# Optimization experiments

Hardware: AMD Instinct MI355X
Metric: run time of the kernel (lower is better)

The kernel has to match this reference:

```python
import jax, jax.numpy as jnp
import numpy as np

H = 16      # numHeads (== numKeyValueHeads since keyValueHeadsPerHead=1)
D = 128     # headDim


def setup_inputs() -> dict:
    key = jax.random.key(0)
    k1, k2, k3 = jax.random.split(key, 3)
    B, S, dim = 2, 2048, 2048
    x = jax.random.normal(k1, (B, S, dim), dtype=jnp.float32)
    # qkvProj: Linear(dim -> (H + 2*H)*D) without bias; torch Linear weight is [out, in]
    Wqkv = jax.random.normal(k2, ((H + 2 * H) * D, dim), dtype=jnp.float32) * 0.02
    # outProj: Linear(H*D -> dim) without bias
    Wout = jax.random.normal(k3, (dim, H * D), dtype=jnp.float32) * 0.02
    return {"x": x, "Wqkv": Wqkv, "Wout": Wout}


def reference(x, Wqkv, Wout):
    B, S, _ = x.shape
    qkv = jnp.einsum('bsd,ed->bse', x, Wqkv)           # [B, S, 3*H*D]
    qkv = qkv.reshape(B, S, 3 * H, D)
    q = qkv[:, :, :H]                                  # [B, S, H, D]
    k = qkv[:, :, H:2 * H]                             # [B, S, H, D]
    v = qkv[:, :, 2 * H:]                              # [B, S, H, D]
    # explicit QK^T / sqrt(d), softmax in fp32, then @ V (keyValueHeadsPerHead=1
    # collapses the group axis, leaving standard per-head attention)
    logits = jnp.einsum('bqhd,bkhd->bhqk', q, k) * (D ** -0.5)
    w = jax.nn.softmax(logits.astype(jnp.float32), axis=-1).astype(logits.dtype)
    out = jnp.einsum('bhqk,bkhd->bqhd', w, v).reshape(B, S, H * D)
    return jnp.einsum('bse,de->bsd', out, Wout)        # outProj
```

## Files before the change

### kernel.cpp

```cpp
#include <hip/hip_runtime.h>

typedef __bf16 bf16x8 __attribute__((ext_vector_type(8)));
typedef _Float16 f16;
typedef f16 f16x8 __attribute__((ext_vector_type(8)));
typedef float f32x4 __attribute__((ext_vector_type(4)));
typedef unsigned short u16;
typedef u16 u16x4 __attribute__((ext_vector_type(4)));

__device__ __forceinline__ u16 f2bf(float f) {
  unsigned u = __builtin_bit_cast(unsigned, f);
  u += 0x7FFFu + ((u >> 16) & 1u);
  return (u16)(u >> 16);
}

#define GLDS16(g, l) __builtin_amdgcn_global_load_lds(                     \
    (const __attribute__((address_space(1))) unsigned int*)(g),            \
    (__attribute__((address_space(3))) unsigned int*)(l), 16, 0, 0)

__device__ __forceinline__ f32x4 mfma16(bf16x8 a, bf16x8 b, f32x4 c) {
  return __builtin_amdgcn_mfma_f32_16x16x32_bf16(a, b, c, 0, 0, 0);
}
__device__ __forceinline__ f32x4 mfma16h(f16x8 a, f16x8 b, f32x4 c) {
  return __builtin_amdgcn_mfma_f32_16x16x32_f16(a, b, c, 0, 0, 0);
}

__global__ void cvt_bf16(const float* __restrict__ src, u16* __restrict__ dst,
                         int n4, int n4s, float scale) {
  int idx = blockIdx.x * blockDim.x + threadIdx.x;
  int stride = gridDim.x * blockDim.x;
  for (int i = idx; i < n4; i += stride) {
    float4 v = ((const float4*)src)[i];
    float sc = (i < n4s) ? scale : 1.0f;
    u16x4 o = { f2bf(v.x * sc), f2bf(v.y * sc), f2bf(v.z * sc), f2bf(v.w * sc) };
    ((u16x4*)dst)[i] = o;
  }
}

__global__ __launch_bounds__(512, 1) void gemm1_qkv(
    const u16* __restrict__ A, const u16* __restrict__ B,
    u16* __restrict__ QK, u16* __restrict__ VT) {
  __shared__ __align__(16) u16 LA[2][16384];
  __shared__ __align__(16) u16 LB[2][16384];
  constexpr int K = 2048;
  const int t = threadIdx.x, lane = t & 63, w = t >> 6;
  const int wm = w >> 2, wn = w & 3;
  const int l15 = lane & 15, lg = lane >> 4;
  const int l7 = l15 & 7;

  const int bid = blockIdx.x;
  const int wg = (bid & 7) * 48 + (bid >> 3);
  const int bx = wg % 24, by = wg / 24;
  const int m0 = by * 256, n0 = bx * 256;

  const int srow = t >> 3;
  const int schunk = (t & 7) ^ (srow & 7);
  const u16* ga = A + (size_t)(m0 + srow) * K + schunk * 8;
  const u16* gb = B + (size_t)(n0 + srow) * K + schunk * 8;

  f32x4 acc[8][4] = {};

#define STG_ALL(kt, bf) do {                                               \
    const int ko_ = (kt) * 64;                                             \
    GLDS16(ga + ko_,            &LA[bf][0]     + t * 8);                   \
    GLDS16(ga + ko_ + 64  * K,  &LA[bf][4096]  + t * 8);                   \
    GLDS16(ga + ko_ + 128 * K,  &LA[bf][8192]  + t * 8);                   \
    GLDS16(ga + ko_ + 192 * K,  &LA[bf][12288] + t * 8);                   \
    GLDS16(gb + ko_,            &LB[bf][0]     + t * 8);                   \
    GLDS16(gb + ko_ + 64  * K,  &LB[bf][4096]  + t * 8);                   \
    GLDS16(gb + ko_ + 128 * K,  &LB[bf][8192]  + t * 8);                   \
    GLDS16(gb + ko_ + 192 * K,  &LB[bf][12288] + t * 8);                   \
  } while (0)
#define BAR() do { __builtin_amdgcn_s_barrier();                           \
                   __builtin_amdgcn_sched_barrier(0); } while (0)

  STG_ALL(0, 0);

#pragma unroll 1
  for (int T = 0; T < 32; ++T) {
    const int bf = T & 1;
    if (T < 31) {
      STG_ALL(T + 1, bf ^ 1);
      asm volatile("s_waitcnt vmcnt(8)" ::: "memory");
    } else {
      asm volatile("s_waitcnt vmcnt(0)" ::: "memory");
    }
    __builtin_amdgcn_sched_barrier(0);
    BAR();

    const u16* la = &LA[bf][0];
    const u16* lb = &LB[bf][0];
    bf16x8 aF[2][4], bF0[2][2], bF1[2][2];

#pragma unroll
    for (int kk = 0; kk < 2; ++kk) {
      const int cp = ((kk * 4 + lg) ^ l7) * 8;
#pragma unroll
      for (int i = 0; i < 4; ++i)
        aF[kk][i] = *(const bf16x8*)&la[(wm * 128 + i * 16 + l15) * 64 + cp];
#pragma unroll
      for (int j = 0; j < 2; ++j)
        bF0[kk][j] = *(const bf16x8*)&lb[(wn * 64 + j * 16 + l15) * 64 + cp];
    }
    __builtin_amdgcn_s_setprio(1);
#pragma unroll
    for (int i = 0; i < 4; ++i)
#pragma unroll
      for (int j = 0; j < 2; ++j)
#pragma unroll
        for (int kk = 0; kk < 2; ++kk)
          acc[i][j] = mfma16(aF[kk][i], bF0[kk][j], acc[i][j]);
    __builtin_amdgcn_s_setprio(0);
    BAR();

#pragma unroll
    for (int kk = 0; kk < 2; ++kk) {
      const int cp = ((kk * 4 + lg) ^ l7) * 8;
#pragma unroll
      for (int j = 0; j < 2; ++j)
        bF1[kk][j] = *(const bf16x8*)&lb[(wn * 64 + 32 + j * 16 + l15) * 64 + cp];
    }
    __builtin_amdgcn_s_setprio(1);
#pragma unroll
    for (int i = 0; i < 4; ++i)
#pragma unroll
      for (int j = 0; j < 2; ++j)
#pragma unroll
        for (int kk = 0; kk < 2; ++kk)
          acc[i][2 + j] = mfma16(aF[kk][i], bF1[kk][j], acc[i][2 + j]);
    __builtin_amdgcn_s_setprio(0);
    BAR();

#pragma unroll
    for (int kk = 0; kk < 2; ++kk) {
      const int cp = ((kk * 4 + lg) ^ l7) * 8;
#pragma unroll
      for (int i = 0; i < 4; ++i)
        aF[kk][i] = *(const bf16x8*)&la[(wm * 128 + 64 + i * 16 + l15) * 64 + cp];
    }
    __builtin_amdgcn_s_setprio(1);
#pragma unroll
    for (int i = 0; i < 4; ++i)
#pragma unroll
      for (int j = 0; j < 2; ++j)
#pragma unroll
        for (int kk = 0; kk < 2; ++kk)
          acc[4 + i][j] = mfma16(aF[kk][i], bF0[kk][j], acc[4 + i][j]);
    __builtin_amdgcn_s_setprio(0);
    BAR();

    __builtin_amdgcn_s_setprio(1);
#pragma unroll
    for (int i = 0; i < 4; ++i)
#pragma unroll
      for (int j = 0; j < 2; ++j)
#pragma unroll
        for (int kk = 0; kk < 2; ++kk)
          acc[4 + i][2 + j] = mfma16(aF[kk][i], bF1[kk][j], acc[4 + i][2 + j]);
    __builtin_amdgcn_s_setprio(0);
    asm volatile("s_waitcnt lgkmcnt(0)" ::: "memory");
    __builtin_amdgcn_sched_barrier(0);
    BAR();
  }
#undef STG_ALL
#undef BAR

  const int rb = m0 + wm * 128 + lg * 4;
  const int cb0 = wn * 64 + l15;
  if (n0 < 4096) {
#pragma unroll
    for (int i = 0; i < 8; ++i)
#pragma unroll
      for (int j = 0; j < 4; ++j) {
        const int row0 = rb + i * 16;
        const int col = n0 + cb0 + j * 16;
#pragma unroll
        for (int jj = 0; jj < 4; ++jj)
          QK[(size_t)(row0 + jj) * 4096 + col] = f2bf(acc[i][j][jj]);
      }
  } else {
#pragma unroll
    for (int i = 0; i < 8; ++i)
#pragma unroll
      for (int j = 0; j < 4; ++j) {
        const int row0 = rb + i * 16;
        const int vcol = (n0 - 4096) + cb0 + j * 16;
        const int bb = row0 >> 11, s = row0 & 2047;
        auto h0 = __builtin_amdgcn_cvt_pkrtz(acc[i][j][0], acc[i][j][1]);
        auto h1 = __builtin_amdgcn_cvt_pkrtz(acc[i][j][2], acc[i][j][3]);
        uint2 pk;
        pk.x = __builtin_bit_cast(unsigned, h0);
        pk.y = __builtin_bit_cast(unsigned, h1);
        *(uint2*)&VT[((size_t)bb * 2048 + vcol) * 2048 + s] = pk;
      }
  }
}

__global__ __launch_bounds__(256, 3) void gemm_bt(
    const u16* __restrict__ A, const u16* __restrict__ B,
    float* __restrict__ C, int M, int N, int K) {
  __shared__ __align__(16) u16 As[2][128 * 32];
  __shared__ __align__(16) u16 Bs[2][128 * 32];
  const int t = threadIdx.x;
  const int lane = t & 63;
  const int w = t >> 6;
  const int wm = w >> 1, wn = w & 1;
  const int l15 = lane & 15, lg = lane >> 4;
  const int m0 = blockIdx.y * 128, n0 = blockIdx.x * 128;
  f32x4 acc[4][4] = {};

  const int srow = t >> 2;
  const int schunk = (t & 3) ^ ((srow >> 1) & 3);
  const u16* ga = A + (size_t)(m0 + srow) * K + schunk * 8;
  const u16* gb = B + (size_t)(n0 + srow) * K + schunk * 8;
  const size_t half = (size_t)64 * K;
  const int ro = l15 * 32 + ((lg ^ ((l15 >> 1) & 3)) * 8);

#define STG(kt, bf) do {                                                   \
    const int ko_ = (kt) * 32;                                             \
    GLDS16(ga + ko_,        &As[bf][0] + t * 8);                           \
    GLDS16(ga + half + ko_, &As[bf][2048] + t * 8);                        \
    GLDS16(gb + ko_,        &Bs[bf][0] + t * 8);                           \
    GLDS16(gb + half + ko_, &Bs[bf][2048] + t * 8);                        \
  } while (0)

#define BODY(bf) do {                                                      \
    const u16* la_ = &As[bf][0];                                           \
    const u16* lb_ = &Bs[bf][0];                                           \
    bf16x8 af[4], bfr[4];                                                  \
    _Pragma("unroll")                                                      \
    for (int i_ = 0; i_ < 4; ++i_)                                         \
      af[i_] = *(const bf16x8*)&la_[(wm * 64 + i_ * 16) * 32 + ro];        \
    _Pragma("unroll")                                                      \
    for (int i_ = 0; i_ < 4; ++i_)                                         \
      bfr[i_] = *(const bf16x8*)&lb_[(wn * 64 + i_ * 16) * 32 + ro];       \
    __builtin_amdgcn_s_setprio(1);                                         \
    _Pragma("unroll")                                                      \
    for (int i_ = 0; i_ < 4; ++i_)                                         \
      _Pragma("unroll")                                                    \
      for (int j_ = 0; j_ < 4; ++j_)                                       \
        acc[i_][j_] = mfma16(af[i_], bfr[j_], acc[i_][j_]);                \
    __builtin_amdgcn_s_setprio(0);                                         \
  } while (0)

  const int NT = K / 32;
  STG(0, 0);
#pragma unroll 1
  for (int T = 0; T < NT - 1; ++T) {
    STG(T + 1, (T + 1) & 1);
    asm volatile("s_waitcnt vmcnt(4)" ::: "memory");
    __builtin_amdgcn_sched_barrier(0);
    __builtin_amdgcn_s_barrier();
    __builtin_amdgcn_sched_barrier(0);
    BODY(T & 1);
    asm volatile("s_waitcnt lgkmcnt(0)" ::: "memory");
    __builtin_amdgcn_sched_barrier(0);
    __builtin_amdgcn_s_barrier();
    __builtin_amdgcn_sched_barrier(0);
  }
  asm volatile("s_waitcnt vmcnt(0)" ::: "memory");
  __builtin_amdgcn_sched_barrier(0);
  __builtin_amdgcn_s_barrier();
  __builtin_amdgcn_sched_barrier(0);
  BODY((NT - 1) & 1);
#undef STG
#undef BODY

  const int rbase = m0 + wm * 64 + (lg << 2);
  const int cbase = n0 + wn * 64 + l15;
#pragma unroll
  for (int i = 0; i < 4; ++i)
#pragma unroll
    for (int j = 0; j < 4; ++j) {
      const int row0 = rbase + i * 16;
      const int col = cbase + j * 16;
#pragma unroll
      for (int jj = 0; jj < 4; ++jj)
        C[(size_t)(row0 + jj) * N + col] = acc[i][j][jj];
    }
}

#define PSTRIDE 72
__global__ __launch_bounds__(512, 1) void attn_fwd(
    const u16* __restrict__ qk, const u16* __restrict__ vt, u16* __restrict__ aout) {
  __shared__ __align__(16) u16 Ks[2][64 * 128];
  __shared__ __align__(16) u16 Vs[2][128 * 64];
  __shared__ __align__(16) u16 Pl[8][32 * PSTRIDE];
  const int t = threadIdx.x, lane = t & 63, w = t >> 6;
  const int bh = blockIdx.x;
  const int b = bh >> 4, h = bh & 15;
  const int q0 = blockIdx.y * 256 + w * 32;
  const int l15 = lane & 15, lg = lane >> 4;

  const u16* qp = qk + (size_t)b * 2048 * 4096 + h * 128;
  const u16* kp = qp + 2048;
  const u16* vtp = vt + (size_t)(b * 16 + h) * 128 * 2048;
  u16* op = aout + (size_t)b * 2048 * 2048 + h * 128;

  int ksoff[2], vsoff[2];
#pragma unroll
  for (int rd = 0; rd < 2; ++rd) {
    const int r = rd * 32 + (t >> 4);
    const int c = (t & 15) ^ (r & 15);
    ksoff[rd] = r * 4096 + c * 8;
    const int rv = rd * 64 + (t >> 3);
    const int cv = (t & 7) ^ (rv & 7);
    vsoff[rd] = rv * 2048 + cv * 8;
  }

  bf16x8 qf[2][4];
#pragma unroll
  for (int mi = 0; mi < 2; ++mi)
#pragma unroll
    for (int kd = 0; kd < 4; ++kd)
      qf[mi][kd] = *(const bf16x8*)&qp[(size_t)(q0 + mi * 16 + l15) * 4096 + kd * 32 + lg * 8];

  f32x4 o[2][8] = {};
  f32x4 lacc[2] = {};
  const f16x8 onesf = {f16(1.f), f16(1.f), f16(1.f), f16(1.f),
                       f16(1.f), f16(1.f), f16(1.f), f16(1.f)};
  u16* pw = &Pl[w][0];

#pragma unroll
  for (int rd = 0; rd < 2; ++rd) {
    GLDS16(kp + ksoff[rd], &Ks[0][0] + rd * 4096 + t * 8);
    GLDS16(vtp + vsoff[rd], &Vs[0][0] + rd * 4096 + t * 8);
  }
  __syncthreads();

  auto tile = [&](const u16* ksb, const u16* vsb, u16* kpre, u16* vpre, int nextit) {
    if (nextit < 32) {
      const size_t kt1 = (size_t)nextit * 64;
#pragma unroll
      for (int rd = 0; rd < 2; ++rd) {
        GLDS16(kp + kt1 * 4096 + ksoff[rd], kpre + rd * 4096 + t * 8);
        GLDS16(vtp + kt1 + vsoff[rd], vpre + rd * 4096 + t * 8);
      }
    }
    f32x4 sf[2][4];
    __builtin_amdgcn_s_setprio(1);
#pragma unroll
    for (int ni = 0; ni < 4; ++ni) {
      const int r = ni * 16 + l15;
      bf16x8 kf[4];
#pragma unroll
      for (int kd = 0; kd < 4; ++kd)
        kf[kd] = *(const bf16x8*)&ksb[r * 128 + (((kd * 4 + lg) ^ l15) * 8)];
#pragma unroll
      for (int mi = 0; mi < 2; ++mi) {
        f32x4 s = {0.f, 0.f, 0.f, 0.f};
        s = mfma16(kf[0], qf[mi][0], s);
        s = mfma16(kf[1], qf[mi][1], s);
        s = mfma16(kf[2], qf[mi][2], s);
        s = mfma16(kf[3], qf[mi][3], s);
        sf[mi][ni] = s;
      }
    }
    __builtin_amdgcn_s_setprio(0);

#pragma unroll
    for (int mi = 0; mi < 2; ++mi)
#pragma unroll
      for (int ni = 0; ni < 4; ++ni) {
        float p0 = exp2f(sf[mi][ni][0]);
        float p1 = exp2f(sf[mi][ni][1]);
        float p2 = exp2f(sf[mi][ni][2]);
        float p3 = exp2f(sf[mi][ni][3]);
        auto h0 = __builtin_amdgcn_cvt_pkrtz(p0, p1);
        auto h1 = __builtin_amdgcn_cvt_pkrtz(p2, p3);
        uint2 wv;
        wv.x = __builtin_bit_cast(unsigned, h0);
        wv.y = __builtin_bit_cast(unsigned, h1);
        *(uint2*)&pw[(mi * 16 + l15) * PSTRIDE + ni * 16 + lg * 4] = wv;
      }

    f16x8 pa[2][2];
#pragma unroll
    for (int mi = 0; mi < 2; ++mi)
#pragma unroll
      for (int ks = 0; ks < 2; ++ks)
        pa[mi][ks] = *(const f16x8*)&pw[(mi * 16 + l15) * PSTRIDE + ks * 32 + lg * 8];
    __builtin_amdgcn_s_setprio(1);
#pragma unroll
    for (int mi = 0; mi < 2; ++mi) {
      lacc[mi] = mfma16h(pa[mi][0], onesf, lacc[mi]);
      lacc[mi] = mfma16h(pa[mi][1], onesf, lacc[mi]);
    }
#pragma unroll
    for (int n2 = 0; n2 < 8; ++n2) {
      const int r = n2 * 16 + l15;
      f16x8 vf0 = *(const f16x8*)&vsb[r * 64 + (((0 * 4 + lg) ^ (l15 & 7)) * 8)];
      f16x8 vf1 = *(const f16x8*)&vsb[r * 64 + (((1 * 4 + lg) ^ (l15 & 7)) * 8)];
#pragma unroll
      for (int mi = 0; mi < 2; ++mi) {
        o[mi][n2] = mfma16h(pa[mi][0], vf0, o[mi][n2]);
        o[mi][n2] = mfma16h(pa[mi][1], vf1, o[mi][n2]);
      }
    }
    __builtin_amdgcn_s_setprio(0);
    __syncthreads();
  };

#pragma unroll 1
  for (int it = 0; it < 32; it += 2) {
    tile(&Ks[0][0], &Vs[0][0], &Ks[1][0], &Vs[1][0], it + 1);
    tile(&Ks[1][0], &Vs[1][0], &Ks[0][0], &Vs[0][0], it + 2);
  }

#pragma unroll
  for (int mi = 0; mi < 2; ++mi)
#pragma unroll
    for (int j = 0; j < 4; ++j) {
      float inv = 1.f / lacc[mi][j];
#pragma unroll
      for (int n2 = 0; n2 < 8; ++n2)
        op[(size_t)(q0 + mi * 16 + lg * 4 + j) * 2048 + n2 * 16 + l15] =
            f2bf(o[mi][n2][j] * inv);
    }
}

extern "C" void kernel_launch(void* const* d_in, const int* in_sizes, int n_in,
                              void* d_out, int out_size, void* d_ws, size_t ws_size,
                              hipStream_t stream) {
  const float* x    = (const float*)d_in[0];
  const float* Wqkv = (const float*)d_in[1];
  const float* Wout = (const float*)d_in[2];
  float* out = (float*)d_out;

  u16* ws = (u16*)d_ws;
  u16* xb    = ws;
  u16* wqkvb = ws + 8388608;
  u16* woutb = ws + 20971520;
  u16* qkbuf = ws + 25165824;
  u16* vtbuf = ws + 41943040;
  u16* aout  = xb;

  const float qscale = 0.08838834764831845f * 1.4426950408889634f;

  cvt_bf16<<<2048, 256, 0, stream>>>(x,    xb,    8388608 / 4, 0, 1.0f);
  cvt_bf16<<<2048, 256, 0, stream>>>(Wqkv, wqkvb, 12582912 / 4, 4194304 / 4, qscale);
  cvt_bf16<<<1024, 256, 0, stream>>>(Wout, woutb, 4194304 / 4, 0, 1.0f);

  gemm1_qkv<<<384, 512, 0, stream>>>(xb, wqkvb, qkbuf, vtbuf);
  attn_fwd<<<dim3(32, 8, 1), 512, 0, stream>>>(qkbuf, vtbuf, aout);
  gemm_bt<<<dim3(16, 32), 256, 0, stream>>>(aout, woutb, out, 4096, 2048, 2048);
}
```

Baseline: 291.6 us.

## Interleave next-tile global-to-LDS loads across the four MFMA phases of the QKV GEMM

Replaces the single bulk prefetch of all eight A/B chunks at the start of each K iteration with staggered issuance: two chunks are issued before each of the four MFMA phases, in the order the next iteration consumes them. Partial vmcnt waits and extra barriers are placed so each chunk is ready before it is read. The aim is to spread memory traffic evenly and overlap it with matrix math rather than stalling on one large wait. The cost is more barriers per iteration and a more fragile ordering; a missed dependency would be a race.

After: 272.2 us. -6.6%, faster.

```diff
diff --git a/kernel.cpp b/kernel.cpp
--- a/kernel.cpp
+++ b/kernel.cpp
@@ -59,84 +59,88 @@
 
   f32x4 acc[8][4] = {};
 
-#define STG_ALL(kt, bf) do {                                               \
-    const int ko_ = (kt) * 64;                                             \
-    GLDS16(ga + ko_,            &LA[bf][0]     + t * 8);                   \
-    GLDS16(ga + ko_ + 64  * K,  &LA[bf][4096]  + t * 8);                   \
-    GLDS16(ga + ko_ + 128 * K,  &LA[bf][8192]  + t * 8);                   \
-    GLDS16(ga + ko_ + 192 * K,  &LA[bf][12288] + t * 8);                   \
-    GLDS16(gb + ko_,            &LB[bf][0]     + t * 8);                   \
-    GLDS16(gb + ko_ + 64  * K,  &LB[bf][4096]  + t * 8);                   \
-    GLDS16(gb + ko_ + 128 * K,  &LB[bf][8192]  + t * 8);                   \
-    GLDS16(gb + ko_ + 192 * K,  &LB[bf][12288] + t * 8);                   \
-  } while (0)
-#define BAR() do { __builtin_amdgcn_s_barrier();                           \
-                   __builtin_amdgcn_sched_barrier(0); } while (0)
-
-  STG_ALL(0, 0);
+#define STG_A(ch, kt, bfi)                                                 \
+    GLDS16(ga + (kt) * 64 + (size_t)(ch) * 64 * K, &LA[bfi][(ch) * 4096] + t * 8)
+#define STG_B(ch, kt, bfi)                                                 \
+    GLDS16(gb + (kt) * 64 + (size_t)(ch) * 64 * K, &LB[bfi][(ch) * 4096] + t * 8)
+
+  STG_A(0, 0, 0); STG_A(2, 0, 0);
+  STG_B(0, 0, 0); STG_B(1, 0, 0); STG_B(2, 0, 0); STG_B(3, 0, 0);
+  STG_A(1, 0, 0); STG_A(3, 0, 0);
+  asm volatile("s_waitcnt vmcnt(2)" ::: "memory");
+  __builtin_amdgcn_s_barrier();
 
 #pragma unroll 1
   for (int T = 0; T < 32; ++T) {
-    const int bf = T & 1;
-    if (T < 31) {
-      STG_ALL(T + 1, bf ^ 1);
-      asm volatile("s_waitcnt vmcnt(8)" ::: "memory");
+    const int p = T & 1, np = p ^ 1;
+    const bool st = (T < 31);
+    const u16* la = &LA[p][0];
+    const u16* lb = &LB[p][0];
+    bf16x8 aF[2][4], bF0[2][2], bF1[2][2];
+
+#pragma unroll
+    for (int kk = 0; kk < 2; ++kk) {
+      const int cp = ((kk * 4 + lg) ^ l7) * 8;
+#pragma unroll
+      for (int i = 0; i < 4; ++i)
+        aF[kk][i] = *(const bf16x8*)&la[(wm * 128 + i * 16 + l15) * 64 + cp];
+#pragma unroll
+      for (int j = 0; j < 2; ++j)
+        bF0[kk][j] = *(const bf16x8*)&lb[(wn * 64 + j * 16 + l15) * 64 + cp];
+    }
+    if (st) { STG_A(0, T + 1, np); STG_A(2, T + 1, np); }
+    __builtin_amdgcn_s_barrier();
+    asm volatile("s_waitcnt lgkmcnt(0)" ::: "memory");
+    __builtin_amdgcn_sched_barrier(0);
+    __builtin_amdgcn_s_setprio(1);
+#pragma unroll
+    for (int i = 0; i < 4; ++i)
+#pragma unroll
+      for (int j = 0; j < 2; ++j)
+#pragma unroll
+        for (int kk = 0; kk < 2; ++kk)
+          acc[i][j] = mfma16(aF[kk][i], bF0[kk][j], acc[i][j]);
+    __builtin_amdgcn_s_setprio(0);
+    __builtin_amdgcn_s_barrier();
+
+#pragma unroll
+    for (int kk = 0; kk < 2; ++kk) {
+      const int cp = ((kk * 4 + lg) ^ l7) * 8;
+#pragma unroll
+      for (int j = 0; j < 2; ++j)
+        bF1[kk][j] = *(const bf16x8*)&lb[(wn * 64 + 32 + j * 16 + l15) * 64 + cp];
+    }
+    if (st) {
+      STG_B(0, T + 1, np); STG_B(1, T + 1, np);
+      asm volatile("s_waitcnt vmcnt(4)" ::: "memory");
     } else {
       asm volatile("s_waitcnt vmcnt(0)" ::: "memory");
     }
-    __builtin_amdgcn_sched_barrier(0);
-    BAR();
-
-    const u16* la = &LA[bf][0];
-    const u16* lb = &LB[bf][0];
-    bf16x8 aF[2][4], bF0[2][2], bF1[2][2];
+    __builtin_amdgcn_s_barrier();
+    asm volatile("s_waitcnt lgkmcnt(0)" ::: "memory");
+    __builtin_amdgcn_sched_barrier(0);
+    __builtin_amdgcn_s_setprio(1);
+#pragma unroll
+    for (int i = 0; i < 4; ++i)
+#pragma unroll
+      for (int j = 0; j < 2; ++j)
+#pragma unroll
+        for (int kk = 0; kk < 2; ++kk)
+          acc[i][2 + j] = mfma16(aF[kk][i], bF1[kk][j], acc[i][2 + j]);
+    __builtin_amdgcn_s_setprio(0);
+    __builtin_amdgcn_s_barrier();
 
 #pragma unroll
     for (int kk = 0; kk < 2; ++kk) {
       const int cp = ((kk * 4 + lg) ^ l7) * 8;
 #pragma unroll
       for (int i = 0; i < 4; ++i)
-        aF[kk][i] = *(const bf16x8*)&la[(wm * 128 + i * 16 + l15) * 64 + cp];
-#pragma unroll
-      for (int j = 0; j < 2; ++j)
-        bF0[kk][j] = *(const bf16x8*)&lb[(wn * 64 + j * 16 + l15) * 64 + cp];
-    }
-    __builtin_amdgcn_s_setprio(1);
-#pragma unroll
-    for (int i = 0; i < 4; ++i)
-#pragma unroll
-      for (int j = 0; j < 2; ++j)
-#pragma unroll
-        for (int kk = 0; kk < 2; ++kk)
-          acc[i][j] = mfma16(aF[kk][i], bF0[kk][j], acc[i][j]);
-    __builtin_amdgcn_s_setprio(0);
-    BAR();
-
-#pragma unroll
-    for (int kk = 0; kk < 2; ++kk) {
-      const int cp = ((kk * 4 + lg) ^ l7) * 8;
-#pragma unroll
-      for (int j = 0; j < 2; ++j)
-        bF1[kk][j] = *(const bf16x8*)&lb[(wn * 64 + 32 + j * 16 + l15) * 64 + cp];
-    }
-    __builtin_amdgcn_s_setprio(1);
-#pragma unroll
-    for (int i = 0; i < 4; ++i)
-#pragma unroll
-      for (int j = 0; j < 2; ++j)
-#pragma unroll
-        for (int kk = 0; kk < 2; ++kk)
-          acc[i][2 + j] = mfma16(aF[kk][i], bF1[kk][j], acc[i][2 + j]);
-    __builtin_amdgcn_s_setprio(0);
-    BAR();
-
-#pragma unroll
-    for (int kk = 0; kk < 2; ++kk) {
-      const int cp = ((kk * 4 + lg) ^ l7) * 8;
-#pragma unroll
-      for (int i = 0; i < 4; ++i)
         aF[kk][i] = *(const bf16x8*)&la[(wm * 128 + 64 + i * 16 + l15) * 64 + cp];
     }
+    if (st) { STG_B(2, T + 1, np); STG_B(3, T + 1, np); }
+    __builtin_amdgcn_s_barrier();
+    asm volatile("s_waitcnt lgkmcnt(0)" ::: "memory");
+    __builtin_amdgcn_sched_barrier(0);
     __builtin_amdgcn_s_setprio(1);
 #pragma unroll
     for (int i = 0; i < 4; ++i)
@@ -146,8 +150,13 @@
         for (int kk = 0; kk < 2; ++kk)
           acc[4 + i][j] = mfma16(aF[kk][i], bF0[kk][j], acc[4 + i][j]);
     __builtin_amdgcn_s_setprio(0);
-    BAR();
-
+    __builtin_amdgcn_s_barrier();
+
+    if (st) {
+      STG_A(1, T + 1, np); STG_A(3, T + 1, np);
+      asm volatile("s_waitcnt vmcnt(2)" ::: "memory");
+    }
+    __builtin_amdgcn_s_barrier();
     __builtin_amdgcn_s_setprio(1);
 #pragma unroll
     for (int i = 0; i < 4; ++i)
@@ -157,12 +166,10 @@
         for (int kk = 0; kk < 2; ++kk)
           acc[4 + i][2 + j] = mfma16(aF[kk][i], bF1[kk][j], acc[4 + i][2 + j]);
     __builtin_amdgcn_s_setprio(0);
-    asm volatile("s_waitcnt lgkmcnt(0)" ::: "memory");
-    __builtin_amdgcn_sched_barrier(0);
-    BAR();
-  }
-#undef STG_ALL
-#undef BAR
+    __builtin_amdgcn_s_barrier();
+  }
+#undef STG_A
+#undef STG_B
 
   const int rb = m0 + wm * 128 + lg * 4;
   const int cb0 = wn * 64 + l15;
```
